# Optimization experiments

Measured on AMD Instinct MI355X. Metric: run time of the kernel, lower is better.

The kernel has to match this reference:

```python
import jax, jax.numpy as jnp
from jax import lax
import numpy as np

K = 31      # avg_pool2d kernel_size
PAD = 15    # avg_pool2d padding
EPS = 1.0
GAMMA = 5.0


def _box_avg(x):
    # Separable 31x31 box filter, stride 1, zero padding 15,
    # count_include_pad=True (PyTorch default) -> always divide by K*K.
    s = lax.reduce_window(x, 0.0, lax.add, (1, 1, K, 1), (1, 1, 1, 1),
                          [(0, 0), (0, 0), (PAD, PAD), (0, 0)])
    s = lax.reduce_window(s, 0.0, lax.add, (1, 1, 1, K), (1, 1, 1, 1),
                          [(0, 0), (0, 0), (0, 0), (PAD, PAD)])
    return s / (K * K)


def setup_inputs() -> dict:
    key = jax.random.key(0)
    k1, k2 = jax.random.split(key)
    shape = (64, 1, 512, 512)  # [B, C, H, W]
    inp = jax.random.uniform(k1, shape, dtype=jnp.float32)
    tgt = jax.random.uniform(k2, shape, dtype=jnp.float32)
    return {"input": inp, "target": tgt}


def reference(input, target):
    weight = 1.0 + GAMMA * jnp.abs(_box_avg(target) - target)
    intersection = jnp.sum(input * target * weight)
    denom = jnp.sum(input * weight) + jnp.sum(target * weight)
    dice = (2.0 * intersection + EPS) / (denom + EPS)
    return 1.0 - dice
```

## Files before the change

### kernel.cpp

```cpp
#include <hip/hip_runtime.h>


#define BATCH 64
#define H     512
#define W     512
#define PADT  16
#define PADB  15
#define HP    (H + PADT + PADB)
#define K1_BLOCKS 2048
#define RB    4
#define K2_BLOCKS 2048

typedef _Float16 half8  __attribute__((ext_vector_type(8)));
typedef float    floatx4 __attribute__((ext_vector_type(4)));

__global__ __launch_bounds__(256) void hrow_kernel(const float* __restrict__ tgt,
                                                   _Float16* __restrict__ hbuf) {
    const int tid  = threadIdx.x;
    const int lane = tid & 63;
    const int wid  = blockIdx.x * 4 + (tid >> 6);
    const int col0 = lane * 8;
    const int r0   = wid * 4;

    const float mL1 = (lane >= 1) ? 1.f : 0.f;
    const float mR1 = (lane <= 62) ? 1.f : 0.f;
    const float mL2 = (lane >= 2) ? 1.f : 0.f;
    const float mR2 = (lane <= 61) ? 1.f : 0.f;

    if (wid < BATCH * 32) {
        const int img = wid >> 5, p = wid & 31;
        if (p < 31) {
            const int row = (p < PADT) ? p : p + H;
            half8 z = {};
            *(half8*)(hbuf + ((size_t)img * HP + row) * W + col0) = z;
        }
    }

    floatx4 va[4][2];
    #pragma unroll
    for (int k = 0; k < 4; ++k) {
        const float* trow = tgt + (size_t)(r0 + k) * W + col0;
        va[k][0] = *(const floatx4*)(trow);
        va[k][1] = *(const floatx4*)(trow + 4);
    }

    #pragma unroll
    for (int k = 0; k < 4; ++k) {
        const float p1 = va[k][0][0];
        const float p2 = p1 + va[k][0][1];
        const float p3 = p2 + va[k][0][2];
        const float p4 = p3 + va[k][0][3];
        const float p5 = p4 + va[k][1][0];
        const float p6 = p5 + va[k][1][1];
        const float p7 = p6 + va[k][1][2];
        const float s  = p7 + va[k][1][3];
        const float f1 = s - p1, f2 = s - p2, f3 = s - p3, f4 = s - p4;
        const float f5 = s - p5, f6 = s - p6, f7 = s - p7;

        const float sL1 = __shfl_up(s, 1, 64);
        const float sR1 = __shfl_down(s, 1, 64);
        const float g1 = __shfl_up(f1, 2, 64);
        const float g2 = __shfl_up(f2, 2, 64);
        const float g3 = __shfl_up(f3, 2, 64);
        const float g4 = __shfl_up(f4, 2, 64);
        const float g5 = __shfl_up(f5, 2, 64);
        const float g6 = __shfl_up(f6, 2, 64);
        const float g7 = __shfl_up(f7, 2, 64);
        const float q1 = __shfl_down(p1, 2, 64);
        const float q2 = __shfl_down(p2, 2, 64);
        const float q3 = __shfl_down(p3, 2, 64);
        const float q4 = __shfl_down(p4, 2, 64);
        const float q5 = __shfl_down(p5, 2, 64);
        const float q6 = __shfl_down(p6, 2, 64);
        const float q7 = __shfl_down(p7, 2, 64);

        const float S3 = fmaf(mL1, sL1, fmaf(mR1, sR1, s));
        half8 hv;
        hv[0] = (_Float16)fmaf(mL2, g1, S3);
        hv[1] = (_Float16)fmaf(mL2, g2, fmaf(mR2, q1, S3));
        hv[2] = (_Float16)fmaf(mL2, g3, fmaf(mR2, q2, S3));
        hv[3] = (_Float16)fmaf(mL2, g4, fmaf(mR2, q3, S3));
        hv[4] = (_Float16)fmaf(mL2, g5, fmaf(mR2, q4, S3));
        hv[5] = (_Float16)fmaf(mL2, g6, fmaf(mR2, q5, S3));
        hv[6] = (_Float16)fmaf(mL2, g7, fmaf(mR2, q6, S3));
        hv[7] = (_Float16)fmaf(mR2, q7, S3);

        const int r = r0 + k;
        *(half8*)(hbuf + ((size_t)(r >> 9) * HP + (r & 511) + PADT) * W + col0) = hv;
    }
}

__global__ __launch_bounds__(256) void main_kernel(const float* __restrict__ tgt,
                                                   const float* __restrict__ inp,
                                                   const _Float16* __restrict__ hbuf,
                                                   float4* __restrict__ partials) {
    const int tid  = threadIdx.x;
    const int lane = tid & 63;
    const int wv   = tid >> 6;
    const int g    = blockIdx.x;
    const int img  = g >> 5;
    const int band = (g & 31) * 4 + wv;
    const int r0   = band * RB;
    const int col0 = lane * 8;

    const float*    timg = tgt  + (size_t)img * H * W;
    const float*    iimg = inp  + (size_t)img * H * W;
    const _Float16* hrp  = hbuf + (size_t)img * HP * W;

    float box[8];
    #pragma unroll
    for (int q = 0; q < 8; ++q) box[q] = 0.f;
    #pragma unroll
    for (int j = 0; j < 31; ++j) {
        const half8 hv = *(const half8*)(hrp + (size_t)(r0 + 1 + j) * W + col0);
        #pragma unroll
        for (int q = 0; q < 8; ++q) box[q] += (float)hv[q];
    }

    const float inv = 1.0f / 961.0f;
    float aI = 0.f, aA = 0.f, aB = 0.f;

    #pragma unroll
    for (int st = 0; st < RB; ++st) {
        const int h = r0 + st;
        if (st > 0) {
            const half8 a = *(const half8*)(hrp + (size_t)(h + 31) * W + col0);
            const half8 s = *(const half8*)(hrp + (size_t)h * W + col0);
            #pragma unroll
            for (int q = 0; q < 8; ++q) box[q] += (float)a[q] - (float)s[q];
        }
        const floatx4 t0 = *(const floatx4*)(timg + (size_t)h * W + col0);
        const floatx4 t1 = *(const floatx4*)(timg + (size_t)h * W + col0 + 4);
        const floatx4 i0 = *(const floatx4*)(iimg + (size_t)h * W + col0);
        const floatx4 i1 = *(const floatx4*)(iimg + (size_t)h * W + col0 + 4);
        const float tv[8] = {t0[0], t0[1], t0[2], t0[3], t1[0], t1[1], t1[2], t1[3]};
        const float iv[8] = {i0[0], i0[1], i0[2], i0[3], i1[0], i1[1], i1[2], i1[3]};

        #pragma unroll
        for (int k = 0; k < 8; ++k) {
            const float wgt = fmaf(5.0f, fabsf(fmaf(box[k], inv, -tv[k])), 1.0f);
            const float tw  = tv[k] * wgt;
            aI = fmaf(iv[k], tw, aI);
            aA = fmaf(iv[k], wgt, aA);
            aB += tw;
        }
    }

    #pragma unroll
    for (int off = 32; off > 0; off >>= 1) {
        aI += __shfl_down(aI, off, 64);
        aA += __shfl_down(aA, off, 64);
        aB += __shfl_down(aB, off, 64);
    }
    __shared__ float sm[12];
    if (lane == 0) { sm[wv] = aI; sm[4 + wv] = aA; sm[8 + wv] = aB; }
    __syncthreads();
    if (tid == 0) {
        float4 o;
        o.x = sm[0] + sm[1] + sm[2] + sm[3];
        o.y = sm[4] + sm[5] + sm[6] + sm[7];
        o.z = sm[8] + sm[9] + sm[10] + sm[11];
        o.w = 0.f;
        partials[g] = o;
    }
}

__global__ __launch_bounds__(1024) void reduce_kernel(const float4* __restrict__ partials,
                                                      float* __restrict__ out) {
    const int tid = threadIdx.x;
    const float4 v0 = partials[tid];
    const float4 v1 = partials[tid + 1024];
    float aI = v0.x + v1.x, aA = v0.y + v1.y, aB = v0.z + v1.z;
    #pragma unroll
    for (int off = 32; off > 0; off >>= 1) {
        aI += __shfl_down(aI, off, 64);
        aA += __shfl_down(aA, off, 64);
        aB += __shfl_down(aB, off, 64);
    }
    __shared__ float s[3][16];
    const int wvx = tid >> 6, ln = tid & 63;
    if (ln == 0) { s[0][wvx] = aI; s[1][wvx] = aA; s[2][wvx] = aB; }
    __syncthreads();
    if (tid == 0) {
        float I = 0.f, A = 0.f, Bv = 0.f;
        #pragma unroll
        for (int k = 0; k < 16; ++k) { I += s[0][k]; A += s[1][k]; Bv += s[2][k]; }
        out[0] = 1.0f - (2.0f * I + 1.0f) / (A + Bv + 1.0f);
    }
}

extern "C" void kernel_launch(void* const* d_in, const int* in_sizes, int n_in,
                              void* d_out, int out_size, void* d_ws, size_t ws_size,
                              hipStream_t stream) {
    const float* inp = (const float*)d_in[0];
    const float* tgt = (const float*)d_in[1];
    float* out = (float*)d_out;

    _Float16* hbuf = (_Float16*)d_ws;
    float4* partials = (float4*)((char*)d_ws + (size_t)BATCH * HP * W * sizeof(_Float16));

    hrow_kernel<<<K1_BLOCKS, 256, 0, stream>>>(tgt, hbuf);
    main_kernel<<<K2_BLOCKS, 256, 0, stream>>>(tgt, inp, hbuf, partials);
    reduce_kernel<<<1, 1024, 0, stream>>>(partials, out);
}
```

Before: 168.9 us.

## Stage fp16 target copy in row pass and double rows per wave

The horizontal-sum kernel now also writes a half-precision copy of the target. The main kernel reads that copy instead of the fp32 target, halving the bytes it reads for the target. The main kernel also maps each wave to 8 rows by 256 columns instead of 4 rows by 512 columns, which lowers how often the 31-row vertical-window halo of the row-sum buffer is re-read. In exchange it adds an extra fp16 write pass and rounds the target values to fp16, which costs some accuracy in the weights and sums.

```diff
diff --git a/kernel.cpp b/kernel.cpp
--- a/kernel.cpp
+++ b/kernel.cpp
@@ -8,14 +8,16 @@
 #define PADB  15
 #define HP    (H + PADT + PADB)
 #define K1_BLOCKS 2048
-#define RB    4
+#define RB    8
 #define K2_BLOCKS 2048
 
 typedef _Float16 half8  __attribute__((ext_vector_type(8)));
+typedef _Float16 half4  __attribute__((ext_vector_type(4)));
 typedef float    floatx4 __attribute__((ext_vector_type(4)));
 
 __global__ __launch_bounds__(256) void hrow_kernel(const float* __restrict__ tgt,
-                                                   _Float16* __restrict__ hbuf) {
+                                                   _Float16* __restrict__ hbuf,
+                                                   _Float16* __restrict__ tbuf) {
     const int tid  = threadIdx.x;
     const int lane = tid & 63;
     const int wid  = blockIdx.x * 4 + (tid >> 6);
@@ -87,34 +89,43 @@
 
         const int r = r0 + k;
         *(half8*)(hbuf + ((size_t)(r >> 9) * HP + (r & 511) + PADT) * W + col0) = hv;
-    }
-}
-
-__global__ __launch_bounds__(256) void main_kernel(const float* __restrict__ tgt,
-                                                   const float* __restrict__ inp,
+
+        half8 tv16;
+        #pragma unroll
+        for (int q = 0; q < 4; ++q) tv16[q] = (_Float16)va[k][0][q];
+        #pragma unroll
+        for (int q = 0; q < 4; ++q) tv16[4 + q] = (_Float16)va[k][1][q];
+        *(half8*)(tbuf + (size_t)r * W + col0) = tv16;
+    }
+}
+
+__global__ __launch_bounds__(256) void main_kernel(const float* __restrict__ inp,
                                                    const _Float16* __restrict__ hbuf,
+                                                   const _Float16* __restrict__ tbuf,
                                                    float4* __restrict__ partials) {
     const int tid  = threadIdx.x;
     const int lane = tid & 63;
     const int wv   = tid >> 6;
-    const int g    = blockIdx.x;
-    const int img  = g >> 5;
-    const int band = (g & 31) * 4 + wv;
+    const int wtid = blockIdx.x * 4 + wv;
+    const int img  = wtid >> 7;
+    const int r    = wtid & 127;
+    const int band = r >> 1;
+    const int half = r & 1;
     const int r0   = band * RB;
-    const int col0 = lane * 8;
-
-    const float*    timg = tgt  + (size_t)img * H * W;
+    const int col0 = half * 256 + lane * 4;
+
     const float*    iimg = inp  + (size_t)img * H * W;
     const _Float16* hrp  = hbuf + (size_t)img * HP * W;
-
-    float box[8];
-    #pragma unroll
-    for (int q = 0; q < 8; ++q) box[q] = 0.f;
+    const _Float16* trp  = tbuf + (size_t)img * H * W;
+
+    float box[4];
+    #pragma unroll
+    for (int q = 0; q < 4; ++q) box[q] = 0.f;
     #pragma unroll
     for (int j = 0; j < 31; ++j) {
-        const half8 hv = *(const half8*)(hrp + (size_t)(r0 + 1 + j) * W + col0);
-        #pragma unroll
-        for (int q = 0; q < 8; ++q) box[q] += (float)hv[q];
+        const half4 hv = *(const half4*)(hrp + (size_t)(r0 + 1 + j) * W + col0);
+        #pragma unroll
+        for (int q = 0; q < 4; ++q) box[q] += (float)hv[q];
     }
 
     const float inv = 1.0f / 961.0f;
@@ -124,24 +135,21 @@
     for (int st = 0; st < RB; ++st) {
         const int h = r0 + st;
         if (st > 0) {
-            const half8 a = *(const half8*)(hrp + (size_t)(h + 31) * W + col0);
-            const half8 s = *(const half8*)(hrp + (size_t)h * W + col0);
+            const half4 a = *(const half4*)(hrp + (size_t)(h + 31) * W + col0);
+            const half4 s = *(const half4*)(hrp + (size_t)h * W + col0);
             #pragma unroll
-            for (int q = 0; q < 8; ++q) box[q] += (float)a[q] - (float)s[q];
+            for (int q = 0; q < 4; ++q) box[q] += (float)a[q] - (float)s[q];
         }
-        const floatx4 t0 = *(const floatx4*)(timg + (size_t)h * W + col0);
-        const floatx4 t1 = *(const floatx4*)(timg + (size_t)h * W + col0 + 4);
-        const floatx4 i0 = *(const floatx4*)(iimg + (size_t)h * W + col0);
-        const floatx4 i1 = *(const floatx4*)(iimg + (size_t)h * W + col0 + 4);
-        const float tv[8] = {t0[0], t0[1], t0[2], t0[3], t1[0], t1[1], t1[2], t1[3]};
-        const float iv[8] = {i0[0], i0[1], i0[2], i0[3], i1[0], i1[1], i1[2], i1[3]};
-
-        #pragma unroll
-        for (int k = 0; k < 8; ++k) {
-            const float wgt = fmaf(5.0f, fabsf(fmaf(box[k], inv, -tv[k])), 1.0f);
-            const float tw  = tv[k] * wgt;
-            aI = fmaf(iv[k], tw, aI);
-            aA = fmaf(iv[k], wgt, aA);
+        const floatx4 iv4 = *(const floatx4*)(iimg + (size_t)h * W + col0);
+        const half4   tv4 = *(const half4*)(trp + (size_t)h * W + col0);
+
+        #pragma unroll
+        for (int k = 0; k < 4; ++k) {
+            const float tv  = (float)tv4[k];
+            const float wgt = fmaf(5.0f, fabsf(fmaf(box[k], inv, -tv)), 1.0f);
+            const float tw  = tv * wgt;
+            aI = fmaf(iv4[k], tw, aI);
+            aA = fmaf(iv4[k], wgt, aA);
             aB += tw;
         }
     }
@@ -161,7 +169,7 @@
         o.y = sm[4] + sm[5] + sm[6] + sm[7];
         o.z = sm[8] + sm[9] + sm[10] + sm[11];
         o.w = 0.f;
-        partials[g] = o;
+        partials[blockIdx.x] = o;
     }
 }
 
@@ -197,9 +205,10 @@
     float* out = (float*)d_out;
 
     _Float16* hbuf = (_Float16*)d_ws;
-    float4* partials = (float4*)((char*)d_ws + (size_t)BATCH * HP * W * sizeof(_Float16));
-
-    hrow_kernel<<<K1_BLOCKS, 256, 0, stream>>>(tgt, hbuf);
-    main_kernel<<<K2_BLOCKS, 256, 0, stream>>>(tgt, inp, hbuf, partials);
+    _Float16* tbuf = (_Float16*)((char*)d_ws + (size_t)BATCH * HP * W * sizeof(_Float16));
+    float4* partials = (float4*)((char*)d_ws + (size_t)BATCH * (HP + H) * W * sizeof(_Float16));
+
+    hrow_kernel<<<K1_BLOCKS, 256, 0, stream>>>(tgt, hbuf, tbuf);
+    main_kernel<<<K2_BLOCKS, 256, 0, stream>>>(inp, hbuf, tbuf, partials);
     reduce_kernel<<<1, 1024, 0, stream>>>(partials, out);
 }
```

Result: faster. 164.1 us (-2.8%).
